# Optimization experiments

Hardware: AMD Instinct MI355X
Metric: run time of the kernel (lower is better)

The kernel has to match this reference:

```python
import jax, jax.numpy as jnp
import numpy as np

N_RBF = 20
CUTOFF = 15.0
N_ATOMS, N_EDGES, D, H = 8192, 262144, 256, 256
D_PAIR = 2 * D + 1 + N_RBF  # 533


def setup_inputs() -> dict:
    key = jax.random.key(0)
    ks = jax.random.split(key, 10)
    s = 1.0 / np.sqrt(H).astype(np.float32)
    return {
        "x": jax.random.normal(ks[0], (N_ATOMS, D), jnp.float32),
        "d_ij": jax.random.uniform(ks[1], (N_EDGES,), jnp.float32, 0.5, CUTOFF),
        "idx_i": jnp.sort(jax.random.randint(ks[2], (N_EDGES,), 0, N_ATOMS)),
        "idx_j": jax.random.randint(ks[3], (N_EDGES,), 0, N_ATOMS),
        "W_in": jax.random.normal(ks[4], (D_PAIR, H), jnp.float32) / np.sqrt(D_PAIR).astype(np.float32),
        "b_in": jnp.zeros((H,), jnp.float32),
        "Ws": jax.random.normal(ks[5], (6, H, H), jnp.float32) * s,
        "bs": jnp.zeros((6, H), jnp.float32),
        "W_out": jax.random.normal(ks[6], (H, 1), jnp.float32) * s,
        "b_out": jnp.zeros((1,), jnp.float32),
    }


def _gaussian_rbf(d):
    # GaussianRBF(20, 15.0): offsets linspace(0, cutoff), width = grid spacing
    offsets = jnp.linspace(0.0, CUTOFF, N_RBF)
    width = offsets[1] - offsets[0]
    coeff = -0.5 / (width * width)
    diff = d[:, None] - offsets  # [E, N_RBF]
    return jnp.exp(coeff * diff * diff)


def reference(x, d_ij, idx_i, idx_j, W_in, b_in, Ws, bs, W_out, b_out):
    n_atoms = x.shape[0]
    rbf = _gaussian_rbf(d_ij)  # [E, 20]
    # per-pair representation: x_i | x_j | rbf(d_ij) | d_ij  -> [E, 533]
    pair = jnp.concatenate([x[idx_i], x[idx_j], rbf, d_ij[:, None]], axis=1)
    h = pair @ W_in + b_in  # pair_and_distance_transform -> [E, 256]
    # build_mlp(H, H, H, 5): 6 linears, SiLU after all but the last
    for l in range(6):
        h = h @ Ws[l] + bs[l]
        if l < 5:
            h = jax.nn.silu(h)
    # DeepSets aggregation: scatter-sum pair messages onto center atom i
    pooled = jax.ops.segment_sum(h, idx_i, num_segments=n_atoms)  # [N, 256]
    out = pooled @ W_out + b_out  # per-atom energy [N, 1]
    return out
```

## Files before the change

### kernel.cpp

```cpp
#include <hip/hip_runtime.h>


typedef _Float16 f16x8 __attribute__((ext_vector_type(8)));
typedef _Float16 f16x4 __attribute__((ext_vector_type(4)));
typedef __fp16   fp16v2 __attribute__((ext_vector_type(2)));
typedef float    f32x4 __attribute__((ext_vector_type(4)));
typedef unsigned int u32x4 __attribute__((ext_vector_type(4)));
typedef unsigned int u32x2 __attribute__((ext_vector_type(2)));

union H8 { f16x8 v; _Float16 h[8]; u32x4 u; };
union H4 { f16x4 v; u32x2 u; };
union H2 { fp16v2 h; unsigned int u; };

#define MFMA16(a, b, c) __builtin_amdgcn_mfma_f32_16x16x32_f16((a), (b), (c), 0, 0, 0)

#define LOG2E 1.44269504088896340736f

#define WS_WP   0u
#define WS_WPI  786432u
#define WS_WPJ  917504u
#define WS_WPR  1048576u
#define WS_XH   1064960u
#define WS_AP   5259264u
#define WS_BP   9453568u

__global__ __launch_bounds__(256) void k_prep(
    const float* __restrict__ x, const float* __restrict__ W_in,
    const float* __restrict__ Ws, const float* __restrict__ b_out,
    _Float16* __restrict__ wp, _Float16* __restrict__ wpi,
    _Float16* __restrict__ wpj, _Float16* __restrict__ wpr,
    _Float16* __restrict__ xh, float* __restrict__ out)
{
  int i = blockIdx.x * 256 + threadIdx.x;
  if (i < 2097152) { xh[i] = (_Float16)x[i]; return; }
  i -= 2097152;
  if (i < 393216) {
    int m = i >> 16, r = i & 65535;
    int j = r & 7, lane = (r >> 3) & 63, ks = (r >> 9) & 7, nt = (r >> 12) & 15;
    int k = ks * 32 + (lane >> 4) * 8 + j, n = nt * 16 + (lane & 15);
    wp[i] = (_Float16)Ws[(m * 256 + k) * 256 + n];
    return;
  }
  i -= 393216;
  if (i < 65536) {
    int j = i & 7, lane = (i >> 3) & 63, ks = (i >> 9) & 7, nt = (i >> 12) & 15;
    int k = ks * 32 + (lane >> 4) * 8 + j, n = nt * 16 + (lane & 15);
    wpi[i] = (_Float16)W_in[k * 256 + n];
    return;
  }
  i -= 65536;
  if (i < 65536) {
    int j = i & 7, lane = (i >> 3) & 63, ks = (i >> 9) & 7, nt = (i >> 12) & 15;
    int k = ks * 32 + (lane >> 4) * 8 + j, n = nt * 16 + (lane & 15);
    wpj[i] = (_Float16)W_in[(256 + k) * 256 + n];
    return;
  }
  i -= 65536;
  if (i < 8192) {
    int j = i & 7, lane = (i >> 3) & 63, nt = (i >> 9) & 15;
    int k = (lane >> 4) * 8 + j, n = nt * 16 + (lane & 15);
    float v = 0.0f;
    if (k < 20)       v = W_in[(512 + k) * 256 + n];
    else if (k == 20) v = W_in[532 * 256 + n];
    wpr[i] = (_Float16)v;
    return;
  }
  i -= 8192;
  if (i < 8192) out[i] = b_out[0];
}

__global__ __launch_bounds__(256) void k_atoms(
    const _Float16* __restrict__ xh,
    const _Float16* __restrict__ wpi, const _Float16* __restrict__ wpj,
    const float* __restrict__ b_in,
    _Float16* __restrict__ AP, _Float16* __restrict__ BP)
{
  const int tid = threadIdx.x;
  const int l = tid & 63, w = tid >> 6;
  const int g = l >> 4, c = l & 15;
  const int which = blockIdx.y;
  const _Float16* wpx = which ? wpj : wpi;
  _Float16* outp = which ? BP : AP;
  const int abase = blockIdx.x * 64;

  f32x4 acc[4][4];
#pragma unroll
  for (int nf = 0; nf < 4; ++nf)
#pragma unroll
    for (int at = 0; at < 4; ++at) acc[nf][at] = (f32x4)0.0f;

#pragma unroll
  for (int ks = 0; ks < 8; ++ks) {
    f16x8 a[4];
#pragma unroll
    for (int nf = 0; nf < 4; ++nf) {
      H8 t; t.u = *(const u32x4*)(wpx + (((w * 4 + nf) * 8 + ks) * 64 + l) * 8);
      a[nf] = t.v;
    }
#pragma unroll
    for (int at = 0; at < 4; ++at) {
      H8 b; b.u = *(const u32x4*)(xh + (abase + at * 16 + c) * 256 + ks * 32 + g * 8);
#pragma unroll
      for (int nf = 0; nf < 4; ++nf)
        acc[nf][at] = MFMA16(a[nf], b.v, acc[nf][at]);
    }
  }

#pragma unroll
  for (int nf = 0; nf < 4; ++nf) {
    const int n = w * 64 + nf * 16 + g * 4;
    f32x4 bias = (f32x4)0.0f;
    if (!which) bias = *(const f32x4*)(b_in + n);
#pragma unroll
    for (int at = 0; at < 4; ++at) {
      const int atom = abase + at * 16 + c;
      const f32x4 t = acc[nf][at] + bias;
      H2 lo, hi;
      lo.h = __builtin_amdgcn_cvt_pkrtz(t[0], t[1]);
      hi.h = __builtin_amdgcn_cvt_pkrtz(t[2], t[3]);
      u32x2 q; q[0] = lo.u; q[1] = hi.u;
      *(u32x2*)(outp + atom * 256 + n) = q;
    }
  }
}

__global__ __launch_bounds__(256, 2) void k_edges(
    const _Float16* __restrict__ AP, const _Float16* __restrict__ BP,
    const int* __restrict__ idx_i, const int* __restrict__ idx_j,
    const float* __restrict__ d_ij,
    const _Float16* __restrict__ wp, const _Float16* __restrict__ wpr,
    const float* __restrict__ bs, const float* __restrict__ W_out,
    float* __restrict__ out)
{
  __shared__ __align__(16) char hb[65536];
  __shared__ float d_lds[128];
  __shared__ int   ii_lds[128];
  __shared__ int   jj_lds[128];
  __shared__ float oacc[128];

  const int tid = threadIdx.x;
  const int l = tid & 63, w = tid >> 6;
  const int g = l >> 4, c = l & 15;
  const int ebase = blockIdx.x * 128;
  const int nb = w * 64;
  const int sw = (c << 4) | ((c & 1) << 8);

  if (tid < 128) {
    ii_lds[tid] = idx_i[ebase + tid];
    jj_lds[tid] = idx_j[ebase + tid];
    d_lds[tid]  = d_ij[ebase + tid];
    oacc[tid]   = 0.0f;
  }
  __syncthreads();

  f32x4 acc[4][8];

  {
    const float STEP = 15.0f / 19.0f;
    const float C2 = (-0.5f / (STEP * STEP)) * LOG2E;
    f16x8 afr[4];
#pragma unroll
    for (int nf = 0; nf < 4; ++nf) {
      H8 t; t.u = *(const u32x4*)(wpr + ((w * 4 + nf) * 64 + l) * 8);
      afr[nf] = t.v;
    }
#pragma unroll
    for (int et = 0; et < 8; ++et) {
      const float d = d_lds[et * 16 + c];
      H8 bb;
#pragma unroll
      for (int j = 0; j < 8; ++j) {
        const int k = g * 8 + j;
        float v = 0.0f;
        if (k < 20)       { const float df = d - (float)k * STEP; v = __builtin_amdgcn_exp2f(C2 * df * df); }
        else if (k == 20) { v = d; }
        bb.h[j] = (_Float16)v;
      }
      const f32x4 z = (f32x4)0.0f;
#pragma unroll
      for (int nf = 0; nf < 4; ++nf)
        acc[nf][et] = MFMA16(afr[nf], bb.v, z);
    }
  }
#pragma unroll
  for (int nf = 0; nf < 4; ++nf) {
    const int n = nb + nf * 16 + g * 4;
    const int obase = n * 2;
#pragma unroll
    for (int et = 0; et < 8; ++et) {
      const int el = et * 16 + c;
      H4 pa, pb, s;
      pa.u = *(const u32x2*)(AP + ii_lds[el] * 256 + n);
      pb.u = *(const u32x2*)(BP + jj_lds[el] * 256 + n);
      H2 lo, hi;
      lo.h = __builtin_amdgcn_cvt_pkrtz(acc[nf][et][0], acc[nf][et][1]);
      hi.h = __builtin_amdgcn_cvt_pkrtz(acc[nf][et][2], acc[nf][et][3]);
      s.u[0] = lo.u; s.u[1] = hi.u;
      s.v = s.v + pa.v + pb.v;
      *(u32x2*)(hb + el * 512 + (obase ^ sw)) = s.u;
    }
  }
  __syncthreads();

  auto mfma_layer = [&](const _Float16* wl, const float* brow) {
#pragma unroll
    for (int nf = 0; nf < 4; ++nf) {
      const f32x4 bias = *(const f32x4*)(brow + nb + nf * 16 + g * 4);
#pragma unroll
      for (int et = 0; et < 8; ++et) acc[nf][et] = bias;
    }
    __builtin_amdgcn_s_setprio(1);
#pragma unroll
    for (int ks = 0; ks < 8; ++ks) {
      f16x8 a[4];
#pragma unroll
      for (int nf = 0; nf < 4; ++nf) {
        H8 t; t.u = *(const u32x4*)(wl + (((w * 4 + nf) * 8 + ks) * 64 + l) * 8);
        a[nf] = t.v;
      }
      const int o = (ks * 64 + g * 16) ^ sw;
#pragma unroll
      for (int et = 0; et < 8; ++et) {
        const int el = et * 16 + c;
        H8 b; b.u = *(const u32x4*)(hb + el * 512 + o);
#pragma unroll
        for (int nf = 0; nf < 4; ++nf)
          acc[nf][et] = MFMA16(a[nf], b.v, acc[nf][et]);
      }
    }
    __builtin_amdgcn_s_setprio(0);
  };

#pragma unroll 1
  for (int ly = 0; ly < 5; ++ly) {
    mfma_layer(wp + ly * 65536, bs + ly * 256);
    __syncthreads();
#pragma unroll
    for (int nf = 0; nf < 4; ++nf) {
      const int n = nb + nf * 16 + g * 4;
      const int obase = n * 2;
#pragma unroll
      for (int et = 0; et < 8; ++et) {
        f32x4 v = acc[nf][et];
#pragma unroll
        for (int j = 0; j < 4; ++j) {
          const float e = __builtin_amdgcn_exp2f(v[j] * -LOG2E);
          v[j] = v[j] * __builtin_amdgcn_rcpf(1.0f + e);
        }
        const int el = et * 16 + c;
        H2 lo, hi;
        lo.h = __builtin_amdgcn_cvt_pkrtz(v[0], v[1]);
        hi.h = __builtin_amdgcn_cvt_pkrtz(v[2], v[3]);
        u32x2 q; q[0] = lo.u; q[1] = hi.u;
        *(u32x2*)(hb + el * 512 + (obase ^ sw)) = q;
      }
    }
    __syncthreads();
  }

  mfma_layer(wp + 5 * 65536, bs + 5 * 256);
  float sum[8];
#pragma unroll
  for (int et = 0; et < 8; ++et) sum[et] = 0.0f;
#pragma unroll
  for (int nf = 0; nf < 4; ++nf) {
    const int n = nb + nf * 16 + g * 4;
    const f32x4 wo = *(const f32x4*)(W_out + n);
#pragma unroll
    for (int et = 0; et < 8; ++et) {
      const f32x4 v = acc[nf][et];
      sum[et] += v[0] * wo[0] + v[1] * wo[1] + v[2] * wo[2] + v[3] * wo[3];
    }
  }
#pragma unroll
  for (int et = 0; et < 8; ++et) {
    float s = sum[et];
    s += __shfl_xor(s, 16, 64);
    s += __shfl_xor(s, 32, 64);
    if (l < 16) atomicAdd(&oacc[et * 16 + l], s);
  }
  __syncthreads();
  if (tid < 128) atomicAdd(out + ii_lds[tid], oacc[tid]);
}

extern "C" void kernel_launch(void* const* d_in, const int* in_sizes, int n_in,
                              void* d_out, int out_size, void* d_ws, size_t ws_size,
                              hipStream_t stream) {
  (void)in_sizes; (void)n_in; (void)out_size; (void)ws_size;
  const float* x     = (const float*)d_in[0];
  const float* d_ij  = (const float*)d_in[1];
  const int*   idx_i = (const int*)d_in[2];
  const int*   idx_j = (const int*)d_in[3];
  const float* W_in  = (const float*)d_in[4];
  const float* b_in  = (const float*)d_in[5];
  const float* Ws    = (const float*)d_in[6];
  const float* bs    = (const float*)d_in[7];
  const float* W_out = (const float*)d_in[8];
  const float* b_out = (const float*)d_in[9];
  float* out = (float*)d_out;
  char* ws = (char*)d_ws;

  _Float16* wp  = (_Float16*)(ws + WS_WP);
  _Float16* wpi = (_Float16*)(ws + WS_WPI);
  _Float16* wpj = (_Float16*)(ws + WS_WPJ);
  _Float16* wpr = (_Float16*)(ws + WS_WPR);
  _Float16* xh  = (_Float16*)(ws + WS_XH);
  _Float16* AP  = (_Float16*)(ws + WS_AP);
  _Float16* BP  = (_Float16*)(ws + WS_BP);

  hipLaunchKernelGGL(k_prep, dim3(10305), dim3(256), 0, stream,
                     x, W_in, Ws, b_out, wp, wpi, wpj, wpr, xh, out);
  hipLaunchKernelGGL(k_atoms, dim3(128, 2), dim3(256), 0, stream,
                     xh, wpi, wpj, b_in, AP, BP);
  hipLaunchKernelGGL(k_edges, dim3(2048), dim3(256), 0, stream,
                     AP, BP, idx_i, idx_j, d_ij, wp, wpr, bs, W_out, out);
}
```

Before: 270.3 us.

## Switch edge MLP to 32x32x16 MFMA with 8 waves split over edges and features

Moves the edge-MLP GEMMs from 16x16x32 to 32x32x16 MFMA tiles and repacks the weights to the matching fragment layout. The block grows to 512 threads, with the 8 waves laid out as 2 edge groups by 4 feature groups, so each wave holds fewer accumulators and more waves are resident to hide latency. The larger tiles also cut LDS activation reads per flop. Trade-offs are a changed LDS swizzle, which could add bank conflicts, and higher register pressure per thread under the 512-thread launch bound.

Measured after the change: 378.1 us. 1.4x slower.

```diff
diff --git a/kernel.cpp b/kernel.cpp
--- a/kernel.cpp
+++ b/kernel.cpp
@@ -5,6 +5,7 @@
 typedef _Float16 f16x4 __attribute__((ext_vector_type(4)));
 typedef __fp16   fp16v2 __attribute__((ext_vector_type(2)));
 typedef float    f32x4 __attribute__((ext_vector_type(4)));
+typedef float    f32x16 __attribute__((ext_vector_type(16)));
 typedef unsigned int u32x4 __attribute__((ext_vector_type(4)));
 typedef unsigned int u32x2 __attribute__((ext_vector_type(2)));
 
@@ -13,6 +14,7 @@
 union H2 { fp16v2 h; unsigned int u; };
 
 #define MFMA16(a, b, c) __builtin_amdgcn_mfma_f32_16x16x32_f16((a), (b), (c), 0, 0, 0)
+#define MFMA32(a, b, c) __builtin_amdgcn_mfma_f32_32x32x16_f16((a), (b), (c), 0, 0, 0)
 
 #define LOG2E 1.44269504088896340736f
 
@@ -36,8 +38,8 @@
   i -= 2097152;
   if (i < 393216) {
     int m = i >> 16, r = i & 65535;
-    int j = r & 7, lane = (r >> 3) & 63, ks = (r >> 9) & 7, nt = (r >> 12) & 15;
-    int k = ks * 32 + (lane >> 4) * 8 + j, n = nt * 16 + (lane & 15);
+    int j = r & 7, lane = (r >> 3) & 63, kstep = (r >> 9) & 15, nt = (r >> 13) & 7;
+    int k = kstep * 16 + (lane >> 5) * 8 + j, n = nt * 32 + (lane & 31);
     wp[i] = (_Float16)Ws[(m * 256 + k) * 256 + n];
     return;
   }
@@ -57,8 +59,8 @@
   }
   i -= 65536;
   if (i < 8192) {
-    int j = i & 7, lane = (i >> 3) & 63, nt = (i >> 9) & 15;
-    int k = (lane >> 4) * 8 + j, n = nt * 16 + (lane & 15);
+    int j = i & 7, lane = (i >> 3) & 63, kstep = (i >> 9) & 1, nt = (i >> 10) & 7;
+    int k = kstep * 16 + (lane >> 5) * 8 + j, n = nt * 32 + (lane & 31);
     float v = 0.0f;
     if (k < 20)       v = W_in[(512 + k) * 256 + n];
     else if (k == 20) v = W_in[532 * 256 + n];
@@ -124,7 +126,7 @@
   }
 }
 
-__global__ __launch_bounds__(256, 2) void k_edges(
+__global__ __launch_bounds__(512, 2) void k_edges(
     const _Float16* __restrict__ AP, const _Float16* __restrict__ BP,
     const int* __restrict__ idx_i, const int* __restrict__ idx_j,
     const float* __restrict__ d_ij,
@@ -140,10 +142,12 @@
 
   const int tid = threadIdx.x;
   const int l = tid & 63, w = tid >> 6;
-  const int g = l >> 4, c = l & 15;
+  const int ge = w >> 2, gn = w & 3;
+  const int e5 = l & 31, h5 = l >> 5;
   const int ebase = blockIdx.x * 128;
-  const int nb = w * 64;
-  const int sw = (c << 4) | ((c & 1) << 8);
+  const int we = ge * 64;
+  const int fb = gn * 64;
+  const int sw = e5 << 4;
 
   if (tid < 128) {
     ii_lds[tid] = idx_i[ebase + tid];
@@ -153,79 +157,92 @@
   }
   __syncthreads();
 
-  f32x4 acc[4][8];
+  f32x16 acc2[2][2];
 
   {
     const float STEP = 15.0f / 19.0f;
     const float C2 = (-0.5f / (STEP * STEP)) * LOG2E;
-    f16x8 afr[4];
-#pragma unroll
-    for (int nf = 0; nf < 4; ++nf) {
-      H8 t; t.u = *(const u32x4*)(wpr + ((w * 4 + nf) * 64 + l) * 8);
-      afr[nf] = t.v;
-    }
-#pragma unroll
-    for (int et = 0; et < 8; ++et) {
-      const float d = d_lds[et * 16 + c];
-      H8 bb;
-#pragma unroll
-      for (int j = 0; j < 8; ++j) {
-        const int k = g * 8 + j;
-        float v = 0.0f;
-        if (k < 20)       { const float df = d - (float)k * STEP; v = __builtin_amdgcn_exp2f(C2 * df * df); }
-        else if (k == 20) { v = d; }
-        bb.h[j] = (_Float16)v;
-      }
-      const f32x4 z = (f32x4)0.0f;
-#pragma unroll
-      for (int nf = 0; nf < 4; ++nf)
-        acc[nf][et] = MFMA16(afr[nf], bb.v, z);
-    }
-  }
-#pragma unroll
-  for (int nf = 0; nf < 4; ++nf) {
-    const int n = nb + nf * 16 + g * 4;
-    const int obase = n * 2;
-#pragma unroll
-    for (int et = 0; et < 8; ++et) {
-      const int el = et * 16 + c;
-      H4 pa, pb, s;
-      pa.u = *(const u32x2*)(AP + ii_lds[el] * 256 + n);
-      pb.u = *(const u32x2*)(BP + jj_lds[el] * 256 + n);
-      H2 lo, hi;
-      lo.h = __builtin_amdgcn_cvt_pkrtz(acc[nf][et][0], acc[nf][et][1]);
-      hi.h = __builtin_amdgcn_cvt_pkrtz(acc[nf][et][2], acc[nf][et][3]);
-      s.u[0] = lo.u; s.u[1] = hi.u;
-      s.v = s.v + pa.v + pb.v;
-      *(u32x2*)(hb + el * 512 + (obase ^ sw)) = s.u;
+    f16x8 afr[2][2];
+#pragma unroll
+    for (int ft = 0; ft < 2; ++ft)
+#pragma unroll
+      for (int ks2 = 0; ks2 < 2; ++ks2) {
+        H8 t; t.u = *(const u32x4*)(wpr + (((gn * 2 + ft) * 2 + ks2) * 64 + l) * 8);
+        afr[ft][ks2] = t.v;
+      }
+#pragma unroll
+    for (int et = 0; et < 2; ++et) {
+      const float d = d_lds[we + et * 32 + e5];
+      H8 bb[2];
+#pragma unroll
+      for (int ks2 = 0; ks2 < 2; ++ks2) {
+#pragma unroll
+        for (int j = 0; j < 8; ++j) {
+          const int k = ks2 * 16 + h5 * 8 + j;
+          float v = 0.0f;
+          if (k < 20)       { const float df = d - (float)k * STEP; v = __builtin_amdgcn_exp2f(C2 * df * df); }
+          else if (k == 20) { v = d; }
+          bb[ks2].h[j] = (_Float16)v;
+        }
+      }
+      const f32x16 z = (f32x16)0.0f;
+#pragma unroll
+      for (int ft = 0; ft < 2; ++ft)
+        acc2[ft][et] = MFMA32(afr[ft][1], bb[1].v, MFMA32(afr[ft][0], bb[0].v, z));
+    }
+  }
+#pragma unroll
+  for (int ft = 0; ft < 2; ++ft) {
+#pragma unroll
+    for (int et = 0; et < 2; ++et) {
+      const int el = we + et * 32 + e5;
+#pragma unroll
+      for (int q = 0; q < 4; ++q) {
+        const int f4 = fb + ft * 32 + q * 8 + h5 * 4;
+        H4 pa, pb, s;
+        pa.u = *(const u32x2*)(AP + ii_lds[el] * 256 + f4);
+        pb.u = *(const u32x2*)(BP + jj_lds[el] * 256 + f4);
+        H2 lo, hi;
+        lo.h = __builtin_amdgcn_cvt_pkrtz(acc2[ft][et][q * 4 + 0], acc2[ft][et][q * 4 + 1]);
+        hi.h = __builtin_amdgcn_cvt_pkrtz(acc2[ft][et][q * 4 + 2], acc2[ft][et][q * 4 + 3]);
+        s.u[0] = lo.u; s.u[1] = hi.u;
+        s.v = s.v + pa.v + pb.v;
+        *(u32x2*)(hb + el * 512 + ((f4 * 2) ^ sw)) = s.u;
+      }
     }
   }
   __syncthreads();
 
   auto mfma_layer = [&](const _Float16* wl, const float* brow) {
 #pragma unroll
-    for (int nf = 0; nf < 4; ++nf) {
-      const f32x4 bias = *(const f32x4*)(brow + nb + nf * 16 + g * 4);
-#pragma unroll
-      for (int et = 0; et < 8; ++et) acc[nf][et] = bias;
+    for (int ft = 0; ft < 2; ++ft) {
+#pragma unroll
+      for (int q = 0; q < 4; ++q) {
+        const f32x4 bq = *(const f32x4*)(brow + fb + ft * 32 + q * 8 + h5 * 4);
+#pragma unroll
+        for (int et = 0; et < 2; ++et) {
+#pragma unroll
+          for (int i2 = 0; i2 < 4; ++i2) acc2[ft][et][q * 4 + i2] = bq[i2];
+        }
+      }
     }
     __builtin_amdgcn_s_setprio(1);
 #pragma unroll
-    for (int ks = 0; ks < 8; ++ks) {
-      f16x8 a[4];
-#pragma unroll
-      for (int nf = 0; nf < 4; ++nf) {
-        H8 t; t.u = *(const u32x4*)(wl + (((w * 4 + nf) * 8 + ks) * 64 + l) * 8);
-        a[nf] = t.v;
-      }
-      const int o = (ks * 64 + g * 16) ^ sw;
-#pragma unroll
-      for (int et = 0; et < 8; ++et) {
-        const int el = et * 16 + c;
+    for (int kstep = 0; kstep < 16; ++kstep) {
+      f16x8 a[2];
+#pragma unroll
+      for (int ft = 0; ft < 2; ++ft) {
+        H8 t; t.u = *(const u32x4*)(wl + (((gn * 2 + ft) * 16 + kstep) * 64 + l) * 8);
+        a[ft] = t.v;
+      }
+      const int o = (kstep * 32 + h5 * 16) ^ sw;
+#pragma unroll
+      for (int et = 0; et < 2; ++et) {
+        const int el = we + et * 32 + e5;
         H8 b; b.u = *(const u32x4*)(hb + el * 512 + o);
 #pragma unroll
-        for (int nf = 0; nf < 4; ++nf)
-          acc[nf][et] = MFMA16(a[nf], b.v, acc[nf][et]);
+        for (int ft = 0; ft < 2; ++ft)
+          acc2[ft][et] = MFMA32(a[ft], b.v, acc2[ft][et]);
       }
     }
     __builtin_amdgcn_s_setprio(0);
@@ -236,48 +253,50 @@
     mfma_layer(wp + ly * 65536, bs + ly * 256);
     __syncthreads();
 #pragma unroll
-    for (int nf = 0; nf < 4; ++nf) {
-      const int n = nb + nf * 16 + g * 4;
-      const int obase = n * 2;
-#pragma unroll
-      for (int et = 0; et < 8; ++et) {
-        f32x4 v = acc[nf][et];
-#pragma unroll
-        for (int j = 0; j < 4; ++j) {
-          const float e = __builtin_amdgcn_exp2f(v[j] * -LOG2E);
-          v[j] = v[j] * __builtin_amdgcn_rcpf(1.0f + e);
+    for (int ft = 0; ft < 2; ++ft) {
+#pragma unroll
+      for (int et = 0; et < 2; ++et) {
+        const int el = we + et * 32 + e5;
+#pragma unroll
+        for (int q = 0; q < 4; ++q) {
+          const int f4 = fb + ft * 32 + q * 8 + h5 * 4;
+          float v0 = acc2[ft][et][q * 4 + 0], v1 = acc2[ft][et][q * 4 + 1];
+          float v2 = acc2[ft][et][q * 4 + 2], v3 = acc2[ft][et][q * 4 + 3];
+          v0 *= __builtin_amdgcn_rcpf(1.0f + __builtin_amdgcn_exp2f(v0 * -LOG2E));
+          v1 *= __builtin_amdgcn_rcpf(1.0f + __builtin_amdgcn_exp2f(v1 * -LOG2E));
+          v2 *= __builtin_amdgcn_rcpf(1.0f + __builtin_amdgcn_exp2f(v2 * -LOG2E));
+          v3 *= __builtin_amdgcn_rcpf(1.0f + __builtin_amdgcn_exp2f(v3 * -LOG2E));
+          H2 lo, hi;
+          lo.h = __builtin_amdgcn_cvt_pkrtz(v0, v1);
+          hi.h = __builtin_amdgcn_cvt_pkrtz(v2, v3);
+          u32x2 qv; qv[0] = lo.u; qv[1] = hi.u;
+          *(u32x2*)(hb + el * 512 + ((f4 * 2) ^ sw)) = qv;
         }
-        const int el = et * 16 + c;
-        H2 lo, hi;
-        lo.h = __builtin_amdgcn_cvt_pkrtz(v[0], v[1]);
-        hi.h = __builtin_amdgcn_cvt_pkrtz(v[2], v[3]);
-        u32x2 q; q[0] = lo.u; q[1] = hi.u;
-        *(u32x2*)(hb + el * 512 + (obase ^ sw)) = q;
       }
     }
     __syncthreads();
   }
 
   mfma_layer(wp + 5 * 65536, bs + 5 * 256);
-  float sum[8];
-#pragma unroll
-  for (int et = 0; et < 8; ++et) sum[et] = 0.0f;
-#pragma unroll
-  for (int nf = 0; nf < 4; ++nf) {
-    const int n = nb + nf * 16 + g * 4;
-    const f32x4 wo = *(const f32x4*)(W_out + n);
-#pragma unroll
-    for (int et = 0; et < 8; ++et) {
-      const f32x4 v = acc[nf][et];
-      sum[et] += v[0] * wo[0] + v[1] * wo[1] + v[2] * wo[2] + v[3] * wo[3];
-    }
-  }
-#pragma unroll
-  for (int et = 0; et < 8; ++et) {
+  float sum[2];
+  sum[0] = 0.0f; sum[1] = 0.0f;
+#pragma unroll
+  for (int ft = 0; ft < 2; ++ft) {
+#pragma unroll
+    for (int q = 0; q < 4; ++q) {
+      const f32x4 wo = *(const f32x4*)(W_out + fb + ft * 32 + q * 8 + h5 * 4);
+#pragma unroll
+      for (int et = 0; et < 2; ++et) {
+        sum[et] += acc2[ft][et][q * 4 + 0] * wo[0] + acc2[ft][et][q * 4 + 1] * wo[1]
+                 + acc2[ft][et][q * 4 + 2] * wo[2] + acc2[ft][et][q * 4 + 3] * wo[3];
+      }
+    }
+  }
+#pragma unroll
+  for (int et = 0; et < 2; ++et) {
     float s = sum[et];
-    s += __shfl_xor(s, 16, 64);
     s += __shfl_xor(s, 32, 64);
-    if (l < 16) atomicAdd(&oacc[et * 16 + l], s);
+    if (l < 32) atomicAdd(&oacc[we + et * 32 + l], s);
   }
   __syncthreads();
   if (tid < 128) atomicAdd(out + ii_lds[tid], oacc[tid]);
@@ -312,6 +331,6 @@
                      x, W_in, Ws, b_out, wp, wpi, wpj, wpr, xh, out);
   hipLaunchKernelGGL(k_atoms, dim3(128, 2), dim3(256), 0, stream,
                      xh, wpi, wpj, b_in, AP, BP);
-  hipLaunchKernelGGL(k_edges, dim3(2048), dim3(256), 0, stream,
+  hipLaunchKernelGGL(k_edges, dim3(2048), dim3(512), 0, stream,
                      AP, BP, idx_i, idx_j, d_ij, wp, wpr, bs, W_out, out);
 }
```
